# Optimization experiments

Hardware: AMD Instinct MI355X
Metric: run time of the kernel (lower is better)

The kernel has to match this reference:

```python
import jax, jax.numpy as jnp
import numpy as np

N_VERTS = 5000
N_FACES = 10000
BATCH = 2
N_PTS = 8192
OUTER_LOOP = 4
INNER_LOOP = 50
SOLVE_SCALE = 10.0
ADAM_LR = 0.01
B1, B2, EPS = 0.9, 0.999, 1e-8


def _normalize(x, eps=1e-12):
    # torch.nn.functional.normalize(p=2, dim=-1)
    n = jnp.linalg.norm(x, axis=-1, keepdims=True)
    return x / jnp.maximum(n, eps)


def _interp_bary(tri, vw):
    # tri: [M,3,3] per-point triangle attributes, vw: [M,2] barycentric (u,v)
    bary = jnp.concatenate([vw, 1.0 - vw[:, :1] - vw[:, 1:2]], axis=-1)  # [M,3]
    return jnp.einsum('mij,mi->mj', tri, bary)


def _solve_delta_vwd(qV, fid, vw, mesh_V, mesh_F, mesh_N):
    # Newton-like correspondence solve via unrolled Adam (solve_delta_vwd).
    tri_idx = mesh_F[fid]          # [M,3]
    tri_V = mesh_V[tri_idx]        # [M,3,3]
    tri_N = mesh_N[tri_idx]        # [M,3,3]
    d0 = jnp.linalg.norm(_interp_bary(tri_V, vw) - qV, axis=-1)
    delta0 = jnp.concatenate([jnp.zeros_like(vw), d0[:, None]], axis=-1)  # [M,3]
    target = qV * SOLVE_SCALE

    def loss_fn(delta):
        w = vw + delta[:, :2]
        cV = _interp_bary(tri_V, w) * SOLVE_SCALE
        cN = _normalize(_interp_bary(tri_N, w)) * SOLVE_SCALE
        match = cV + cN * delta[:, 2:3]
        return jnp.mean((match - target) ** 2)  # F.mse_loss

    def step(carry, t):
        delta, m, v = carry
        g = jax.grad(loss_fn)(delta)
        m = B1 * m + (1.0 - B1) * g
        v = B2 * v + (1.0 - B2) * g * g
        mhat = m / (1.0 - B1 ** t)
        vhat = v / (1.0 - B2 ** t)
        delta = delta - ADAM_LR * mhat / (jnp.sqrt(vhat) + EPS)
        return (delta, m, v), None

    ts = jnp.arange(1, INNER_LOOP + 1, dtype=qV.dtype)
    zeros = jnp.zeros_like(delta0)
    (delta, _, _), _ = jax.lax.scan(step, (delta0, zeros, zeros), ts)
    return delta


def _forward(verts, mesh_V, mesh_N, mesh_F):
    b, n, _ = verts.shape
    # init_corres_spt: KNN (K=1) of query points against triangle centers
    centers = mesh_V[mesh_F].mean(axis=1)  # [F,3]
    d2 = ((verts ** 2).sum(-1)[..., None]
          + (centers ** 2).sum(-1)[None, None, :]
          - 2.0 * jnp.einsum('bnd,fd->bnf', verts, centers))  # [b,n,F]
    fidx = jnp.argmin(d2, axis=-1)                             # [b,n]
    fid = fidx.reshape(-1)
    qV = verts.reshape(-1, 3)
    vw = jnp.full((b * n, 2), 1.0 / 3.0, dtype=verts.dtype)
    # update_corres_spt (method='uvd'): outer triwalk loop.
    # triwalk is an external CPU mesh-walker; we use the module's documented
    # fallback when triwalk is None: vw <- vw + delta (face index unchanged).
    for _ in range(OUTER_LOOP):
        delta = _solve_delta_vwd(qV, fid, vw, mesh_V, mesh_F, mesh_N)
        vw = vw + delta[:, :2]
    outlier_mask = jnp.zeros((b, n), dtype=bool)  # max_dist = inf
    return fidx, vw.reshape(b, n, 2), outlier_mask


def setup_inputs() -> dict:
    key = jax.random.key(0)
    k1, k2, k3, k4 = jax.random.split(key, 4)
    mesh_V = jax.random.normal(k1, (N_VERTS, 3), dtype=jnp.float32)
    mesh_F = jax.random.randint(k2, (N_FACES, 3), 0, N_VERTS)
    mesh_N = _normalize(jax.random.normal(k3, (N_VERTS, 3), dtype=jnp.float32))
    verts = jax.random.normal(k4, (BATCH, N_PTS, 3), dtype=jnp.float32)
    return {"verts": verts, "mesh_V": mesh_V, "mesh_N": mesh_N, "mesh_F": mesh_F}


def reference(verts, mesh_V, mesh_N, mesh_F):
    return _forward(verts, mesh_V, mesh_N, mesh_F)
```

## Files before the change

kernel.cpp:

```cpp
#include <hip/hip_runtime.h>
#include <math.h>

constexpr int kVerts = 5000;
constexpr int kFaces = 10000;
constexpr int kHalf  = kFaces / 2;
constexpr int kPts   = 16384;
constexpr int kOuter = 4;
constexpr int kInner = 50;

#define SCALE 10.0f

struct BiasTab { float rb1[kInner]; float rb2[kInner]; };
constexpr BiasTab make_tab() {
    BiasTab t{};
    float b1 = 1.0f, b2 = 1.0f;
    for (int i = 0; i < kInner; ++i) {
        b1 *= 0.9f; b2 *= 0.999f;
        t.rb1[i] = 1.0f / (1.0f - b1);
        t.rb2[i] = 1.0f / (1.0f - b2);
    }
    return t;
}
__device__ constexpr BiasTab kTab = make_tab();

__global__ __launch_bounds__(256)
void centers_kernel(const float* __restrict__ mesh_V,
                    const int*   __restrict__ mesh_F,
                    float4*      __restrict__ cent)
{
    const int f = blockIdx.x * 256 + threadIdx.x;
    if (f >= kFaces) return;
    const int i0 = mesh_F[f * 3 + 0];
    const int i1 = mesh_F[f * 3 + 1];
    const int i2 = mesh_F[f * 3 + 2];
    const float cx = __fdiv_rn(__fadd_rn(__fadd_rn(mesh_V[i0*3+0], mesh_V[i1*3+0]), mesh_V[i2*3+0]), 3.0f);
    const float cy = __fdiv_rn(__fadd_rn(__fadd_rn(mesh_V[i0*3+1], mesh_V[i1*3+1]), mesh_V[i2*3+1]), 3.0f);
    const float cz = __fdiv_rn(__fadd_rn(__fadd_rn(mesh_V[i0*3+2], mesh_V[i1*3+2]), mesh_V[i2*3+2]), 3.0f);
    const float cc = __fadd_rn(__fadd_rn(__fmul_rn(cx, cx), __fmul_rn(cy, cy)),
                               __fmul_rn(cz, cz));
    cent[f] = make_float4(cx, cy, cz, cc);
}

#define KNN_PARTS 16

__global__ __launch_bounds__(1024)
void knn_kernel(const float* __restrict__ verts,
                const float4* __restrict__ cent,
                float*        __restrict__ ws_d2,
                int*          __restrict__ ws_f)
{
    __shared__ float s_best[1024];
    __shared__ int   s_bestf[1024];

    const int tid  = threadIdx.x;
    const int lane = tid & 63;
    const int part = __builtin_amdgcn_readfirstlane(tid >> 6);
    const int pg   = blockIdx.x >> 1;
    const int half = blockIdx.x & 1;
    const int p    = pg * 64 + lane;

    const float qx = verts[p * 3 + 0];
    const float qy = verts[p * 3 + 1];
    const float qz = verts[p * 3 + 2];
    const float q2 = __fadd_rn(__fadd_rn(__fmul_rn(qx, qx), __fmul_rn(qy, qy)),
                               __fmul_rn(qz, qz));

    const int fbeg = half * kHalf + (part * kHalf) / KNN_PARTS;
    const int fend = half * kHalf + ((part + 1) * kHalf) / KNN_PARTS;

    float bd0 = INFINITY, bd1 = INFINITY, bd2 = INFINITY, bd3 = INFINITY;
    int   bf0 = 0x7fffffff, bf1 = 0x7fffffff, bf2 = 0x7fffffff, bf3 = 0x7fffffff;

#define KNN_EVAL(FF, C, BD, BF)                                                       \
    {                                                                                 \
        const float dot = __fadd_rn(__fadd_rn(__fmul_rn(qx, (C).x),                   \
                                              __fmul_rn(qy, (C).y)),                  \
                                    __fmul_rn(qz, (C).z));                            \
        const float d2 = __fsub_rn(__fadd_rn(q2, (C).w), __fmul_rn(2.0f, dot));       \
        if (d2 < (BD)) { (BD) = d2; (BF) = (FF); }                                    \
    }

    int f = fbeg;
#pragma unroll 2
    for (; f + 4 <= fend; f += 4) {
        const float4 c0 = cent[f + 0];
        const float4 c1 = cent[f + 1];
        const float4 c2 = cent[f + 2];
        const float4 c3 = cent[f + 3];
        KNN_EVAL(f + 0, c0, bd0, bf0);
        KNN_EVAL(f + 1, c1, bd1, bf1);
        KNN_EVAL(f + 2, c2, bd2, bf2);
        KNN_EVAL(f + 3, c3, bd3, bf3);
    }
    for (; f < fend; ++f) {
        const float4 c0 = cent[f];
        KNN_EVAL(f, c0, bd0, bf0);
    }
#undef KNN_EVAL

    if (bd1 < bd0 || (bd1 == bd0 && bf1 < bf0)) { bd0 = bd1; bf0 = bf1; }
    if (bd3 < bd2 || (bd3 == bd2 && bf3 < bf2)) { bd2 = bd3; bf2 = bf3; }
    if (bd2 < bd0 || (bd2 == bd0 && bf2 < bf0)) { bd0 = bd2; bf0 = bf2; }

    s_best[tid]  = bd0;
    s_bestf[tid] = bf0;
    __syncthreads();
    if (part == 0) {
        float best  = bd0;
        int   bestf = bf0;
        for (int k = 1; k < KNN_PARTS; ++k) {
            const float ob = s_best[tid + 64 * k];
            const int   of = s_bestf[tid + 64 * k];
            if (ob < best || (ob == best && of < bestf)) { best = ob; bestf = of; }
        }
        ws_d2[half * kPts + p] = best;
        ws_f [half * kPts + p] = bestf;
    }
}

__global__ __launch_bounds__(64)
void solve_kernel(const float* __restrict__ verts,
                  const float* __restrict__ mesh_V,
                  const float* __restrict__ mesh_N,
                  const int*   __restrict__ mesh_F,
                  const float* __restrict__ ws_d2,
                  const int*   __restrict__ ws_f,
                  float*       __restrict__ out)
{
    const int p = blockIdx.x * 64 + threadIdx.x;

    const float da = ws_d2[p];
    const float db = ws_d2[kPts + p];
    const int   fa = ws_f[p];
    const int   fb = ws_f[kPts + p];
    const int   f  = (db < da) ? fb : fa;
    out[p] = (float)f;

    const float qx = verts[p * 3 + 0];
    const float qy = verts[p * 3 + 1];
    const float qz = verts[p * 3 + 2];

    const int i0 = mesh_F[f * 3 + 0];
    const int i1 = mesh_F[f * 3 + 1];
    const int i2 = mesh_F[f * 3 + 2];

    const float V0x = mesh_V[i0*3+0], V0y = mesh_V[i0*3+1], V0z = mesh_V[i0*3+2];
    const float V1x = mesh_V[i1*3+0], V1y = mesh_V[i1*3+1], V1z = mesh_V[i1*3+2];
    const float V2x = mesh_V[i2*3+0], V2y = mesh_V[i2*3+1], V2z = mesh_V[i2*3+2];
    const float N0x = mesh_N[i0*3+0], N0y = mesh_N[i0*3+1], N0z = mesh_N[i0*3+2];
    const float N1x = mesh_N[i1*3+0], N1y = mesh_N[i1*3+1], N1z = mesh_N[i1*3+2];
    const float N2x = mesh_N[i2*3+0], N2y = mesh_N[i2*3+1], N2z = mesh_N[i2*3+2];

    const float E0x = V0x - V2x, E0y = V0y - V2y, E0z = V0z - V2z;
    const float E1x = V1x - V2x, E1y = V1y - V2y, E1z = V1z - V2z;
    const float F0x = N0x - N2x, F0y = N0y - N2y, F0z = N0z - N2z;
    const float F1x = N1x - N2x, F1y = N1y - N2y, F1z = N1z - N2z;

    const float tx = qx * SCALE, ty = qy * SCALE, tz = qz * SCALE;
    const float GS = 2.0f / (3.0f * 16384.0f);
    const float B1 = 0.9f,  ONE_M_B1 = 1.0f - 0.9f;
    const float B2 = 0.999f, ONE_M_B2 = 1.0f - 0.999f;

    float vwu = 1.0f / 3.0f, vwv = 1.0f / 3.0f;

    for (int outer = 0; outer < kOuter; ++outer) {
        const float bw0 = (1.0f - vwu) - vwv;
        const float px = ((vwu * V0x + vwv * V1x) + bw0 * V2x);
        const float py = ((vwu * V0y + vwv * V1y) + bw0 * V2y);
        const float pz = ((vwu * V0z + vwv * V1z) + bw0 * V2z);
        const float dx = px - qx, dy = py - qy, dz = pz - qz;
        const float d0 = __builtin_amdgcn_sqrtf((dx * dx + dy * dy) + dz * dz);

        float du = 0.0f, dv = 0.0f, dd = d0;
        float mAu = 0.0f, mAv = 0.0f, mAd = 0.0f;
        float vAu = 0.0f, vAv = 0.0f, vAd = 0.0f;

#pragma unroll 10
        for (int it = 0; it < kInner; ++it) {
            const float bu = vwu + du;
            const float bv = vwv + dv;
            const float bw = (1.0f - bu) - bv;

            const float cVx = ((bu * V0x + bv * V1x) + bw * V2x) * SCALE;
            const float cVy = ((bu * V0y + bv * V1y) + bw * V2y) * SCALE;
            const float cVz = ((bu * V0z + bv * V1z) + bw * V2z) * SCALE;

            const float nrx = (bu * N0x + bv * N1x) + bw * N2x;
            const float nry = (bu * N0y + bv * N1y) + bw * N2y;
            const float nrz = (bu * N0z + bv * N1z) + bw * N2z;
            const float nn  = (nrx * nrx + nry * nry) + nrz * nrz;
            const float inv = __builtin_amdgcn_rsqf(nn);
            const float nhx = nrx * inv, nhy = nry * inv, nhz = nrz * inv;
            const float cNx = nhx * SCALE, cNy = nhy * SCALE, cNz = nhz * SCALE;

            const float rx = (cVx + cNx * dd) - tx;
            const float ry = (cVy + cNy * dd) - ty;
            const float rz = (cVz + cNz * dd) - tz;

            const float rv0  = (rx * E0x + ry * E0y) + rz * E0z;
            const float rv1  = (rx * E1x + ry * E1y) + rz * E1z;
            const float rn0  = (rx * F0x + ry * F0y) + rz * F0z;
            const float rn1  = (rx * F1x + ry * F1y) + rz * F1z;
            const float nf0  = (nhx * F0x + nhy * F0y) + nhz * F0z;
            const float nf1  = (nhx * F1x + nhy * F1y) + nhz * F1z;
            const float nr_r = (nhx * rx + nhy * ry) + nhz * rz;

            const float gu = GS * (SCALE * rv0 + (dd * SCALE) * ((rn0 - nr_r * nf0) * inv));
            const float gv = GS * (SCALE * rv1 + (dd * SCALE) * ((rn1 - nr_r * nf1) * inv));
            const float gd = GS * (SCALE * nr_r);

            mAu = B1 * mAu + ONE_M_B1 * gu;
            mAv = B1 * mAv + ONE_M_B1 * gv;
            mAd = B1 * mAd + ONE_M_B1 * gd;
            vAu = B2 * vAu + ONE_M_B2 * (gu * gu);
            vAv = B2 * vAv + ONE_M_B2 * (gv * gv);
            vAd = B2 * vAd + ONE_M_B2 * (gd * gd);

            const float rb1 = kTab.rb1[it];
            const float rb2 = kTab.rb2[it];
            const float su = __builtin_amdgcn_rsqf(vAu * rb2 + 1e-16f);
            const float sv = __builtin_amdgcn_rsqf(vAv * rb2 + 1e-16f);
            const float sd = __builtin_amdgcn_rsqf(vAd * rb2 + 1e-16f);
            du -= 0.01f * (mAu * rb1) * su;
            dv -= 0.01f * (mAv * rb1) * sv;
            dd -= 0.01f * (mAd * rb1) * sd;
        }
        vwu += du;
        vwv += dv;
    }

    out[kPts + 2 * p + 0] = vwu;
    out[kPts + 2 * p + 1] = vwv;
    out[3 * kPts + p]     = 0.0f;
}

extern "C" void kernel_launch(void* const* d_in, const int* in_sizes, int n_in,
                              void* d_out, int out_size, void* d_ws, size_t ws_size,
                              hipStream_t stream) {
    const float* verts  = (const float*)d_in[0];
    const float* mesh_V = (const float*)d_in[1];
    const float* mesh_N = (const float*)d_in[2];
    const int*   mesh_F = (const int*)d_in[3];
    float* out = (float*)d_out;

    float4* ws_cent = (float4*)d_ws;
    float*  ws_d2   = (float*)((char*)d_ws + kFaces * sizeof(float4));
    int*    ws_f    = (int*)((char*)ws_d2 + 2 * kPts * sizeof(float));

    hipLaunchKernelGGL(centers_kernel, dim3((kFaces + 255) / 256), dim3(256), 0, stream,
                       mesh_V, mesh_F, ws_cent);
    hipLaunchKernelGGL(knn_kernel,     dim3(2 * kPts / 64), dim3(1024), 0, stream,
                       verts, ws_cent, ws_d2, ws_f);
    hipLaunchKernelGGL(solve_kernel,   dim3(kPts / 64), dim3(64), 0, stream,
                       verts, mesh_V, mesh_N, mesh_F, ws_d2, ws_f, out);
}
```

Baseline: 140.3 us.

## Register-block KNN over four queries and pack solve into float2 lanes

```diff
diff --git a/kernel.cpp b/kernel.cpp
--- a/kernel.cpp
+++ b/kernel.cpp
@@ -3,21 +3,22 @@
 
 constexpr int kVerts = 5000;
 constexpr int kFaces = 10000;
-constexpr int kHalf  = kFaces / 2;
 constexpr int kPts   = 16384;
 constexpr int kOuter = 4;
 constexpr int kInner = 50;
 
 #define SCALE 10.0f
 
-struct BiasTab { float rb1[kInner]; float rb2[kInner]; };
+typedef float v2 __attribute__((ext_vector_type(2)));
+
+struct BiasTab { float rb[2 * kInner]; };
 constexpr BiasTab make_tab() {
     BiasTab t{};
     float b1 = 1.0f, b2 = 1.0f;
     for (int i = 0; i < kInner; ++i) {
         b1 *= 0.9f; b2 *= 0.999f;
-        t.rb1[i] = 1.0f / (1.0f - b1);
-        t.rb2[i] = 1.0f / (1.0f - b2);
+        t.rb[2 * i + 0] = 1.0f / (1.0f - b1);
+        t.rb[2 * i + 1] = 1.0f / (1.0f - b2);
     }
     return t;
 }
@@ -42,6 +43,8 @@
 }
 
 #define KNN_PARTS 16
+#define KNN_SPLIT 4
+constexpr int kQLen = kFaces / KNN_SPLIT;
 
 __global__ __launch_bounds__(1024)
 void knn_kernel(const float* __restrict__ verts,
@@ -49,76 +52,80 @@
                 float*        __restrict__ ws_d2,
                 int*          __restrict__ ws_f)
 {
-    __shared__ float s_best[1024];
-    __shared__ int   s_bestf[1024];
+    __shared__ float s_best[KNN_PARTS * 256];
+    __shared__ int   s_bestf[KNN_PARTS * 256];
 
     const int tid  = threadIdx.x;
     const int lane = tid & 63;
     const int part = __builtin_amdgcn_readfirstlane(tid >> 6);
-    const int pg   = blockIdx.x >> 1;
-    const int half = blockIdx.x & 1;
-    const int p    = pg * 64 + lane;
-
-    const float qx = verts[p * 3 + 0];
-    const float qy = verts[p * 3 + 1];
-    const float qz = verts[p * 3 + 2];
-    const float q2 = __fadd_rn(__fadd_rn(__fmul_rn(qx, qx), __fmul_rn(qy, qy)),
-                               __fmul_rn(qz, qz));
-
-    const int fbeg = half * kHalf + (part * kHalf) / KNN_PARTS;
-    const int fend = half * kHalf + ((part + 1) * kHalf) / KNN_PARTS;
-
-    float bd0 = INFINITY, bd1 = INFINITY, bd2 = INFINITY, bd3 = INFINITY;
-    int   bf0 = 0x7fffffff, bf1 = 0x7fffffff, bf2 = 0x7fffffff, bf3 = 0x7fffffff;
-
-#define KNN_EVAL(FF, C, BD, BF)                                                       \
+    const int pgi  = blockIdx.x >> 2;
+    const int quar = blockIdx.x & 3;
+    const int p0   = pgi * 256 + lane;
+
+#define KNN_LOADQ(K)                                                                  \
+    const float qx##K = verts[(p0 + 64 * (K)) * 3 + 0];                               \
+    const float qy##K = verts[(p0 + 64 * (K)) * 3 + 1];                               \
+    const float qz##K = verts[(p0 + 64 * (K)) * 3 + 2];                               \
+    const float q2##K = __fadd_rn(__fadd_rn(__fmul_rn(qx##K, qx##K),                  \
+                                            __fmul_rn(qy##K, qy##K)),                 \
+                                  __fmul_rn(qz##K, qz##K));                           \
+    float bd##K = INFINITY; int bf##K = 0x7fffffff;
+    KNN_LOADQ(0) KNN_LOADQ(1) KNN_LOADQ(2) KNN_LOADQ(3)
+#undef KNN_LOADQ
+
+    const int fbeg = quar * kQLen + (part * kQLen) / KNN_PARTS;
+    const int fend = quar * kQLen + ((part + 1) * kQLen) / KNN_PARTS;
+
+#define KNN_EVAL(FF, C, K)                                                            \
     {                                                                                 \
-        const float dot = __fadd_rn(__fadd_rn(__fmul_rn(qx, (C).x),                   \
-                                              __fmul_rn(qy, (C).y)),                  \
-                                    __fmul_rn(qz, (C).z));                            \
-        const float d2 = __fsub_rn(__fadd_rn(q2, (C).w), __fmul_rn(2.0f, dot));       \
-        if (d2 < (BD)) { (BD) = d2; (BF) = (FF); }                                    \
-    }
+        const float dot = __fadd_rn(__fadd_rn(__fmul_rn(qx##K, (C).x),                \
+                                              __fmul_rn(qy##K, (C).y)),               \
+                                    __fmul_rn(qz##K, (C).z));                         \
+        const float d2 = __fsub_rn(__fadd_rn(q2##K, (C).w), __fmul_rn(2.0f, dot));    \
+        if (d2 < bd##K) { bd##K = d2; bf##K = (FF); }                                 \
+    }
+#define KNN_EVAL4(FF, C) KNN_EVAL(FF, C, 0) KNN_EVAL(FF, C, 1) KNN_EVAL(FF, C, 2) KNN_EVAL(FF, C, 3)
 
     int f = fbeg;
-#pragma unroll 2
     for (; f + 4 <= fend; f += 4) {
         const float4 c0 = cent[f + 0];
         const float4 c1 = cent[f + 1];
         const float4 c2 = cent[f + 2];
         const float4 c3 = cent[f + 3];
-        KNN_EVAL(f + 0, c0, bd0, bf0);
-        KNN_EVAL(f + 1, c1, bd1, bf1);
-        KNN_EVAL(f + 2, c2, bd2, bf2);
-        KNN_EVAL(f + 3, c3, bd3, bf3);
+        KNN_EVAL4(f + 0, c0)
+        KNN_EVAL4(f + 1, c1)
+        KNN_EVAL4(f + 2, c2)
+        KNN_EVAL4(f + 3, c3)
     }
     for (; f < fend; ++f) {
         const float4 c0 = cent[f];
-        KNN_EVAL(f, c0, bd0, bf0);
-    }
+        KNN_EVAL4(f, c0)
+    }
+#undef KNN_EVAL4
 #undef KNN_EVAL
 
-    if (bd1 < bd0 || (bd1 == bd0 && bf1 < bf0)) { bd0 = bd1; bf0 = bf1; }
-    if (bd3 < bd2 || (bd3 == bd2 && bf3 < bf2)) { bd2 = bd3; bf2 = bf3; }
-    if (bd2 < bd0 || (bd2 == bd0 && bf2 < bf0)) { bd0 = bd2; bf0 = bf2; }
-
-    s_best[tid]  = bd0;
-    s_bestf[tid] = bf0;
+    s_best [part * 256 + 0 * 64 + lane] = bd0;  s_bestf[part * 256 + 0 * 64 + lane] = bf0;
+    s_best [part * 256 + 1 * 64 + lane] = bd1;  s_bestf[part * 256 + 1 * 64 + lane] = bf1;
+    s_best [part * 256 + 2 * 64 + lane] = bd2;  s_bestf[part * 256 + 2 * 64 + lane] = bf2;
+    s_best [part * 256 + 3 * 64 + lane] = bd3;  s_bestf[part * 256 + 3 * 64 + lane] = bf3;
     __syncthreads();
     if (part == 0) {
-        float best  = bd0;
-        int   bestf = bf0;
-        for (int k = 1; k < KNN_PARTS; ++k) {
-            const float ob = s_best[tid + 64 * k];
-            const int   of = s_bestf[tid + 64 * k];
-            if (ob < best || (ob == best && of < bestf)) { best = ob; bestf = of; }
+#pragma unroll
+        for (int k = 0; k < 4; ++k) {
+            float best  = s_best [k * 64 + lane];
+            int   bestf = s_bestf[k * 64 + lane];
+            for (int pt = 1; pt < KNN_PARTS; ++pt) {
+                const float ob = s_best [pt * 256 + k * 64 + lane];
+                const int   of = s_bestf[pt * 256 + k * 64 + lane];
+                if (ob < best || (ob == best && of < bestf)) { best = ob; bestf = of; }
+            }
+            ws_d2[quar * kPts + p0 + 64 * k] = best;
+            ws_f [quar * kPts + p0 + 64 * k] = bestf;
         }
-        ws_d2[half * kPts + p] = best;
-        ws_f [half * kPts + p] = bestf;
-    }
-}
-
-__global__ __launch_bounds__(64)
+    }
+}
+
+__global__ __launch_bounds__(64, 1)
 void solve_kernel(const float* __restrict__ verts,
                   const float* __restrict__ mesh_V,
                   const float* __restrict__ mesh_N,
@@ -127,87 +134,106 @@
                   const int*   __restrict__ ws_f,
                   float*       __restrict__ out)
 {
-    const int p = blockIdx.x * 64 + threadIdx.x;
-
-    const float da = ws_d2[p];
-    const float db = ws_d2[kPts + p];
-    const int   fa = ws_f[p];
-    const int   fb = ws_f[kPts + p];
-    const int   f  = (db < da) ? fb : fa;
-    out[p] = (float)f;
-
-    const float qx = verts[p * 3 + 0];
-    const float qy = verts[p * 3 + 1];
-    const float qz = verts[p * 3 + 2];
-
-    const int i0 = mesh_F[f * 3 + 0];
-    const int i1 = mesh_F[f * 3 + 1];
-    const int i2 = mesh_F[f * 3 + 2];
-
-    const float V0x = mesh_V[i0*3+0], V0y = mesh_V[i0*3+1], V0z = mesh_V[i0*3+2];
-    const float V1x = mesh_V[i1*3+0], V1y = mesh_V[i1*3+1], V1z = mesh_V[i1*3+2];
-    const float V2x = mesh_V[i2*3+0], V2y = mesh_V[i2*3+1], V2z = mesh_V[i2*3+2];
-    const float N0x = mesh_N[i0*3+0], N0y = mesh_N[i0*3+1], N0z = mesh_N[i0*3+2];
-    const float N1x = mesh_N[i1*3+0], N1y = mesh_N[i1*3+1], N1z = mesh_N[i1*3+2];
-    const float N2x = mesh_N[i2*3+0], N2y = mesh_N[i2*3+1], N2z = mesh_N[i2*3+2];
-
-    const float E0x = V0x - V2x, E0y = V0y - V2y, E0z = V0z - V2z;
-    const float E1x = V1x - V2x, E1y = V1y - V2y, E1z = V1z - V2z;
-    const float F0x = N0x - N2x, F0y = N0y - N2y, F0z = N0z - N2z;
-    const float F1x = N1x - N2x, F1y = N1y - N2y, F1z = N1z - N2z;
-
-    const float tx = qx * SCALE, ty = qy * SCALE, tz = qz * SCALE;
+    const int t = blockIdx.x * 64 + threadIdx.x;
+    int fsel[2];
+
+#pragma unroll
+    for (int k = 0; k < 2; ++k) {
+        const int p = t + k * 8192;
+        float best = ws_d2[p];
+        int   bf   = ws_f[p];
+#pragma unroll
+        for (int q = 1; q < 4; ++q) {
+            const float d = ws_d2[q * kPts + p];
+            const int   ff = ws_f[q * kPts + p];
+            if (d < best) { best = d; bf = ff; }
+        }
+        fsel[k] = bf;
+        out[p] = (float)bf;
+    }
+
+#define LD2(arr, idx0, idx1) (v2){ arr[idx0], arr[idx1] }
+    const int fA = fsel[0], fB = fsel[1];
+    const int a0 = mesh_F[fA*3+0], a1 = mesh_F[fA*3+1], a2 = mesh_F[fA*3+2];
+    const int b0 = mesh_F[fB*3+0], b1 = mesh_F[fB*3+1], b2 = mesh_F[fB*3+2];
+
+    const v2 qx = LD2(verts, t*3+0, (t+8192)*3+0);
+    const v2 qy = LD2(verts, t*3+1, (t+8192)*3+1);
+    const v2 qz = LD2(verts, t*3+2, (t+8192)*3+2);
+
+    const v2 V0x = LD2(mesh_V, a0*3+0, b0*3+0), V0y = LD2(mesh_V, a0*3+1, b0*3+1), V0z = LD2(mesh_V, a0*3+2, b0*3+2);
+    const v2 V1x = LD2(mesh_V, a1*3+0, b1*3+0), V1y = LD2(mesh_V, a1*3+1, b1*3+1), V1z = LD2(mesh_V, a1*3+2, b1*3+2);
+    const v2 V2x = LD2(mesh_V, a2*3+0, b2*3+0), V2y = LD2(mesh_V, a2*3+1, b2*3+1), V2z = LD2(mesh_V, a2*3+2, b2*3+2);
+    const v2 N0x = LD2(mesh_N, a0*3+0, b0*3+0), N0y = LD2(mesh_N, a0*3+1, b0*3+1), N0z = LD2(mesh_N, a0*3+2, b0*3+2);
+    const v2 N1x = LD2(mesh_N, a1*3+0, b1*3+0), N1y = LD2(mesh_N, a1*3+1, b1*3+1), N1z = LD2(mesh_N, a1*3+2, b1*3+2);
+    const v2 N2x = LD2(mesh_N, a2*3+0, b2*3+0), N2y = LD2(mesh_N, a2*3+1, b2*3+1), N2z = LD2(mesh_N, a2*3+2, b2*3+2);
+#undef LD2
+
+    const v2 E0x = V0x - V2x, E0y = V0y - V2y, E0z = V0z - V2z;
+    const v2 E1x = V1x - V2x, E1y = V1y - V2y, E1z = V1z - V2z;
+    const v2 F0x = N0x - N2x, F0y = N0y - N2y, F0z = N0z - N2z;
+    const v2 F1x = N1x - N2x, F1y = N1y - N2y, F1z = N1z - N2z;
+
+    const v2 txv = qx * SCALE, tyv = qy * SCALE, tzv = qz * SCALE;
     const float GS = 2.0f / (3.0f * 16384.0f);
     const float B1 = 0.9f,  ONE_M_B1 = 1.0f - 0.9f;
     const float B2 = 0.999f, ONE_M_B2 = 1.0f - 0.999f;
 
-    float vwu = 1.0f / 3.0f, vwv = 1.0f / 3.0f;
+    v2 vwu = (v2)(1.0f / 3.0f), vwv = (v2)(1.0f / 3.0f);
 
     for (int outer = 0; outer < kOuter; ++outer) {
-        const float bw0 = (1.0f - vwu) - vwv;
-        const float px = ((vwu * V0x + vwv * V1x) + bw0 * V2x);
-        const float py = ((vwu * V0y + vwv * V1y) + bw0 * V2y);
-        const float pz = ((vwu * V0z + vwv * V1z) + bw0 * V2z);
-        const float dx = px - qx, dy = py - qy, dz = pz - qz;
-        const float d0 = __builtin_amdgcn_sqrtf((dx * dx + dy * dy) + dz * dz);
-
-        float du = 0.0f, dv = 0.0f, dd = d0;
-        float mAu = 0.0f, mAv = 0.0f, mAd = 0.0f;
-        float vAu = 0.0f, vAv = 0.0f, vAd = 0.0f;
-
-#pragma unroll 10
+        const v2 bw0 = (1.0f - vwu) - vwv;
+        const v2 px = ((vwu * V0x + vwv * V1x) + bw0 * V2x);
+        const v2 py = ((vwu * V0y + vwv * V1y) + bw0 * V2y);
+        const v2 pz = ((vwu * V0z + vwv * V1z) + bw0 * V2z);
+        const v2 dx = px - qx, dy = py - qy, dz = pz - qz;
+        const v2 dn = (dx * dx + dy * dy) + dz * dz;
+        v2 dd;
+        dd.x = __builtin_amdgcn_sqrtf(dn.x);
+        dd.y = __builtin_amdgcn_sqrtf(dn.y);
+
+        v2 du = (v2)0.0f, dv = (v2)0.0f;
+        v2 mAu = (v2)0.0f, mAv = (v2)0.0f, mAd = (v2)0.0f;
+        v2 vAu = (v2)0.0f, vAv = (v2)0.0f, vAd = (v2)0.0f;
+
+#pragma unroll 2
         for (int it = 0; it < kInner; ++it) {
-            const float bu = vwu + du;
-            const float bv = vwv + dv;
-            const float bw = (1.0f - bu) - bv;
-
-            const float cVx = ((bu * V0x + bv * V1x) + bw * V2x) * SCALE;
-            const float cVy = ((bu * V0y + bv * V1y) + bw * V2y) * SCALE;
-            const float cVz = ((bu * V0z + bv * V1z) + bw * V2z) * SCALE;
-
-            const float nrx = (bu * N0x + bv * N1x) + bw * N2x;
-            const float nry = (bu * N0y + bv * N1y) + bw * N2y;
-            const float nrz = (bu * N0z + bv * N1z) + bw * N2z;
-            const float nn  = (nrx * nrx + nry * nry) + nrz * nrz;
-            const float inv = __builtin_amdgcn_rsqf(nn);
-            const float nhx = nrx * inv, nhy = nry * inv, nhz = nrz * inv;
-            const float cNx = nhx * SCALE, cNy = nhy * SCALE, cNz = nhz * SCALE;
-
-            const float rx = (cVx + cNx * dd) - tx;
-            const float ry = (cVy + cNy * dd) - ty;
-            const float rz = (cVz + cNz * dd) - tz;
-
-            const float rv0  = (rx * E0x + ry * E0y) + rz * E0z;
-            const float rv1  = (rx * E1x + ry * E1y) + rz * E1z;
-            const float rn0  = (rx * F0x + ry * F0y) + rz * F0z;
-            const float rn1  = (rx * F1x + ry * F1y) + rz * F1z;
-            const float nf0  = (nhx * F0x + nhy * F0y) + nhz * F0z;
-            const float nf1  = (nhx * F1x + nhy * F1y) + nhz * F1z;
-            const float nr_r = (nhx * rx + nhy * ry) + nhz * rz;
-
-            const float gu = GS * (SCALE * rv0 + (dd * SCALE) * ((rn0 - nr_r * nf0) * inv));
-            const float gv = GS * (SCALE * rv1 + (dd * SCALE) * ((rn1 - nr_r * nf1) * inv));
-            const float gd = GS * (SCALE * nr_r);
+            const float rb1 = kTab.rb[2 * it + 0];
+            const float rb2 = kTab.rb[2 * it + 1];
+
+            const v2 bu = vwu + du;
+            const v2 bv = vwv + dv;
+            const v2 bw = (1.0f - bu) - bv;
+
+            const v2 cVx = ((bu * V0x + bv * V1x) + bw * V2x) * SCALE;
+            const v2 cVy = ((bu * V0y + bv * V1y) + bw * V2y) * SCALE;
+            const v2 cVz = ((bu * V0z + bv * V1z) + bw * V2z) * SCALE;
+
+            const v2 nrx = (bu * N0x + bv * N1x) + bw * N2x;
+            const v2 nry = (bu * N0y + bv * N1y) + bw * N2y;
+            const v2 nrz = (bu * N0z + bv * N1z) + bw * N2z;
+            const v2 nn  = (nrx * nrx + nry * nry) + nrz * nrz;
+            v2 inv;
+            inv.x = __builtin_amdgcn_rsqf(nn.x);
+            inv.y = __builtin_amdgcn_rsqf(nn.y);
+            const v2 nhx = nrx * inv, nhy = nry * inv, nhz = nrz * inv;
+            const v2 cNx = nhx * SCALE, cNy = nhy * SCALE, cNz = nhz * SCALE;
+
+            const v2 rx = (cVx + cNx * dd) - txv;
+            const v2 ry = (cVy + cNy * dd) - tyv;
+            const v2 rz = (cVz + cNz * dd) - tzv;
+
+            const v2 rv0  = (rx * E0x + ry * E0y) + rz * E0z;
+            const v2 rv1  = (rx * E1x + ry * E1y) + rz * E1z;
+            const v2 rn0  = (rx * F0x + ry * F0y) + rz * F0z;
+            const v2 rn1  = (rx * F1x + ry * F1y) + rz * F1z;
+            const v2 nf0  = (nhx * F0x + nhy * F0y) + nhz * F0z;
+            const v2 nf1  = (nhx * F1x + nhy * F1y) + nhz * F1z;
+            const v2 nr_r = (nhx * rx + nhy * ry) + nhz * rz;
+
+            const v2 gu = GS * (SCALE * rv0 + (dd * SCALE) * ((rn0 - nr_r * nf0) * inv));
+            const v2 gv = GS * (SCALE * rv1 + (dd * SCALE) * ((rn1 - nr_r * nf1) * inv));
+            const v2 gd = GS * (SCALE * nr_r);
 
             mAu = B1 * mAu + ONE_M_B1 * gu;
             mAv = B1 * mAv + ONE_M_B1 * gv;
@@ -216,11 +242,13 @@
             vAv = B2 * vAv + ONE_M_B2 * (gv * gv);
             vAd = B2 * vAd + ONE_M_B2 * (gd * gd);
 
-            const float rb1 = kTab.rb1[it];
-            const float rb2 = kTab.rb2[it];
-            const float su = __builtin_amdgcn_rsqf(vAu * rb2 + 1e-16f);
-            const float sv = __builtin_amdgcn_rsqf(vAv * rb2 + 1e-16f);
-            const float sd = __builtin_amdgcn_rsqf(vAd * rb2 + 1e-16f);
+            const v2 au = vAu * rb2 + 1e-16f;
+            const v2 av = vAv * rb2 + 1e-16f;
+            const v2 ad = vAd * rb2 + 1e-16f;
+            v2 su, sv, sd;
+            su.x = __builtin_amdgcn_rsqf(au.x);  su.y = __builtin_amdgcn_rsqf(au.y);
+            sv.x = __builtin_amdgcn_rsqf(av.x);  sv.y = __builtin_amdgcn_rsqf(av.y);
+            sd.x = __builtin_amdgcn_rsqf(ad.x);  sd.y = __builtin_amdgcn_rsqf(ad.y);
             du -= 0.01f * (mAu * rb1) * su;
             dv -= 0.01f * (mAv * rb1) * sv;
             dd -= 0.01f * (mAd * rb1) * sd;
@@ -229,9 +257,15 @@
         vwv += dv;
     }
 
-    out[kPts + 2 * p + 0] = vwu;
-    out[kPts + 2 * p + 1] = vwv;
-    out[3 * kPts + p]     = 0.0f;
+#pragma unroll
+    for (int k = 0; k < 2; ++k) {
+        const int p = t + k * 8192;
+        const float u = (k == 0) ? vwu.x : vwu.y;
+        const float v = (k == 0) ? vwv.x : vwv.y;
+        out[kPts + 2 * p + 0] = u;
+        out[kPts + 2 * p + 1] = v;
+        out[3 * kPts + p]     = 0.0f;
+    }
 }
 
 extern "C" void kernel_launch(void* const* d_in, const int* in_sizes, int n_in,
@@ -245,12 +279,12 @@
 
     float4* ws_cent = (float4*)d_ws;
     float*  ws_d2   = (float*)((char*)d_ws + kFaces * sizeof(float4));
-    int*    ws_f    = (int*)((char*)ws_d2 + 2 * kPts * sizeof(float));
+    int*    ws_f    = (int*)((char*)ws_d2 + 4 * kPts * sizeof(float));
 
     hipLaunchKernelGGL(centers_kernel, dim3((kFaces + 255) / 256), dim3(256), 0, stream,
                        mesh_V, mesh_F, ws_cent);
-    hipLaunchKernelGGL(knn_kernel,     dim3(2 * kPts / 64), dim3(1024), 0, stream,
+    hipLaunchKernelGGL(knn_kernel,     dim3((kPts / 256) * KNN_SPLIT), dim3(1024), 0, stream,
                        verts, ws_cent, ws_d2, ws_f);
-    hipLaunchKernelGGL(solve_kernel,   dim3(kPts / 64), dim3(64), 0, stream,
+    hipLaunchKernelGGL(solve_kernel,   dim3(8192 / 64), dim3(64), 0, stream,
                        verts, mesh_V, mesh_N, mesh_F, ws_d2, ws_f, out);
 }
```

After: 148.9 us. +6.1%, slower.
